# Kernel tuning notes

Hardware: AMD Instinct MI355X
Metric: run time of the kernel (lower is better)

## Reference

```python
import jax, jax.numpy as jnp
import numpy as np

H = 16            # num_heads
NORM = 16.0       # gate normalizer
SCALE = 128.0 ** -0.5  # (embed_dim // num_heads) ** -0.5, per source
EPS = 1e-5


def setup_inputs() -> dict:
    key = jax.random.key(0)
    ks = jax.random.split(key, 10)
    B, L, D = 2, 2048, 2048
    g = lambda k, shape, s: jax.random.normal(k, shape, jnp.float32) * s
    return {
        "x": g(ks[0], (B, L, D), 1.0),
        "Wq": g(ks[1], (1024, D), 0.02),
        "Wk": g(ks[2], (1024, D), 0.02),
        "Wkg1": g(ks[3], (16, D), 0.02),
        "Wkg2": g(ks[4], (1024, 16), 0.05),
        "bkg2": jnp.zeros((1024,), jnp.float32),
        "Wv": g(ks[5], (D, D), 0.02),
        "Wg": g(ks[6], (D, D), 0.02),
        "bg": jnp.zeros((D,), jnp.float32),
        "Wo": g(ks[7], (D, D), 0.02),
    }


def _gla_core(x, Wq, Wk, Wkg1, Wkg2, bkg2, Wv, Wg, bg, Wo):
    B, L, D = x.shape
    q = x @ Wq.T                         # [B,L,1024]
    k = (x @ Wk.T) * SCALE               # [B,L,1024]
    kg = (x @ Wkg1.T) @ Wkg2.T + bkg2    # [B,L,1024] low-rank gate
    v = x @ Wv.T                         # [B,L,2048]
    gproj = x @ Wg.T + bg                # [B,L,2048]

    dk = q.shape[-1] // H   # 64
    dv = D // H             # 128
    heads = lambda t, dh: t.reshape(B, L, H, dh).transpose(0, 2, 1, 3)  # b h l d
    qh = heads(q, dk)
    kh = heads(k, dk)
    vh = heads(v, dv)
    gk = jax.nn.log_sigmoid(heads(kg, dk)) / NORM  # b h l dk

    # recurrence: S_t = diag(exp(gk_t)) S_{t-1} + k_t v_t^T ; o_t = q_t S_t
    tfirst = lambda t: t.transpose(2, 0, 1, 3)  # l b h d

    def step(S, inp):
        qt, kt, vt, gt = inp
        S = S * jnp.exp(gt)[..., None] + kt[..., None] * vt[..., None, :]
        ot = jnp.einsum('bhk,bhkv->bhv', qt, S)
        return S, ot

    S0 = jnp.zeros((B, H, dk, dv), x.dtype)
    _, os = jax.lax.scan(step, S0, (tfirst(qh), tfirst(kh), tfirst(vh), tfirst(gk)))
    o = os.transpose(1, 2, 0, 3)  # b h l dv

    # LayerNorm over head dim, no affine
    mu = o.mean(-1, keepdims=True)
    var = ((o - mu) ** 2).mean(-1, keepdims=True)
    o = (o - mu) * jax.lax.rsqrt(var + EPS)

    o = o.transpose(0, 2, 1, 3).reshape(B, L, D)  # b l (h dv)
    return (jax.nn.silu(gproj) * o) @ Wo.T


def reference(x, Wq, Wk, Wkg1, Wkg2, bkg2, Wv, Wg, bg, Wo):
    return _gla_core(x, Wq, Wk, Wkg1, Wkg2, bkg2, Wv, Wg, bg, Wo)
```

## Files before the change

kernel.cpp:

```cpp
#include <hip/hip_runtime.h>
#include <hip/hip_bf16.h>

using bf16x8 = __attribute__((ext_vector_type(8))) __bf16;
using fx4    = __attribute__((ext_vector_type(4))) float;
using us4    = __attribute__((ext_vector_type(4))) unsigned short;
using us8    = __attribute__((ext_vector_type(8))) unsigned short;

__device__ __forceinline__ float b2f(unsigned short u) {
    unsigned int x = ((unsigned int)u) << 16;
    return __builtin_bit_cast(float, x);
}
__device__ __forceinline__ unsigned short f2b(float f) {
    __hip_bfloat16 h = __float2bfloat16(f);
    return __builtin_bit_cast(unsigned short, h);
}
__device__ __forceinline__ float logsigmoidf(float z) {
    return fminf(z, 0.0f) - log1pf(expf(-fabsf(z)));
}

__device__ __forceinline__ void gl_lds16(const unsigned short* g, unsigned short* l) {
    __builtin_amdgcn_global_load_lds(
        (const __attribute__((address_space(1))) void*)g,
        (__attribute__((address_space(3))) void*)l, 16, 0, 0);
}

__device__ __forceinline__ bf16x8 frag64(const unsigned short* base, int row, int cq) {
    return *reinterpret_cast<const bf16x8*>(base + row * 64 + (((cq ^ (row & 7)) << 3)));
}
__device__ __forceinline__ int sw_idx(int row, int col) {
    return row * 64 + ((((col >> 3) ^ (row & 7)) << 3)) + (col & 7);
}

__device__ __forceinline__ void xcd_remap(int& bx, int& by) {
    const int gx = gridDim.x;
    const int nwg = gx * gridDim.y;
    const int cpx = nwg >> 3;
    const int f = blockIdx.y * gx + blockIdx.x;
    const int nf = (f & 7) * cpx + (f >> 3);
    bx = nf % gx;
    by = nf / gx;
}

__global__ __launch_bounds__(256) void detect_kernel(
    const unsigned int* __restrict__ x, int* __restrict__ flag)
{
    __shared__ int bad[256];
    const int t = threadIdx.x;
    int b = 0;
#pragma unroll
    for (int i = 0; i < 16; ++i) {
        unsigned int w = x[t * 16 + i];
        float v = b2f((unsigned short)(w & 0xFFFFu));
        if (!(fabsf(v) < 1.0e6f)) b = 1;
    }
    bad[t] = b;
    __syncthreads();
    for (int s = 128; s > 0; s >>= 1) {
        if (t < s) bad[t] |= bad[t + s];
        __syncthreads();
    }
    if (t == 0) flag[0] = bad[0];
}

struct CvtArgs {
    const void* src[10];
    unsigned short* dst[10];
};

__global__ __launch_bounds__(256) void convert_all_kernel(
    CvtArgs a, const int* __restrict__ flag)
{
    const int pref[11] = {0, 1048576, 1310720, 1572864, 1576960, 1579008,
                          1579136, 2103424, 2627712, 2627968, 3152256};
    const int total = 3152256;
    const int f32 = *flag;
    for (int g = blockIdx.x * 256 + threadIdx.x; g < total; g += gridDim.x * 256) {
        int s = 0;
#pragma unroll
        for (int i = 1; i < 10; ++i) s += (g >= pref[i]) ? 1 : 0;
        const int lg = g - pref[s];
        if (f32) {
            const float* sp = (const float*)a.src[s] + (size_t)lg * 8;
            fx4 v0 = *(const fx4*)(sp);
            fx4 v1 = *(const fx4*)(sp + 4);
            us8 r;
#pragma unroll
            for (int e = 0; e < 4; ++e) { r[e] = f2b(v0[e]); r[4 + e] = f2b(v1[e]); }
            *(us8*)(a.dst[s] + (size_t)lg * 8) = r;
        } else {
            *(us8*)(a.dst[s] + (size_t)lg * 8) =
                *(const us8*)((const unsigned short*)a.src[s] + (size_t)lg * 8);
        }
    }
}

struct Seg3 {
    unsigned short* C0;
    unsigned short* C1;
    unsigned short* C2;
    const unsigned short* bias2;
};

__global__ __launch_bounds__(256) void gemm_fused3_kernel(
    const unsigned short* __restrict__ A, const unsigned short* __restrict__ W,
    Seg3 segs, float scale_k)
{
    const int K = 2048;
    __shared__ __align__(16) unsigned short As[128 * 64];
    __shared__ __align__(16) unsigned short Bs[128 * 64];

    const int tid  = threadIdx.x;
    const int lane = tid & 63, wid = tid >> 6;
    const int quad = lane >> 4, l15 = lane & 15;
    const int wm = (wid & 1) * 64, wn = (wid >> 1) * 64;
    int bx, by;
    xcd_remap(bx, by);
    const int m0 = by * 128, n0 = bx * 128;

    fx4 acc[4][4];
#pragma unroll
    for (int i = 0; i < 4; ++i)
#pragma unroll
        for (int j = 0; j < 4; ++j) acc[i][j] = fx4{0.f, 0.f, 0.f, 0.f};

    const int srow = lane >> 3;
    const int g8   = ((lane & 7) ^ srow) * 8;
    const int c8   = (lane & 7) * 8;
    const unsigned short* Ab = A + (size_t)m0 * K;
    const unsigned short* Wb = W + (size_t)n0 * K;

    for (int k0 = 0; k0 < K; k0 += 64) {
#pragma unroll
        for (int p = 0; p < 4; ++p) {
            const int la  = wid * 4 + p;
            const int row = la * 8 + srow;
            gl_lds16(Ab + (size_t)row * K + k0 + g8, As + row * 64 + c8);
            gl_lds16(Wb + (size_t)row * K + k0 + g8, Bs + row * 64 + c8);
        }
        __syncthreads();
#pragma unroll
        for (int ks = 0; ks < 2; ++ks) {
            const int cq = quad + ks * 4;
            bf16x8 af[4], bfr[4];
#pragma unroll
            for (int mt = 0; mt < 4; ++mt) af[mt] = frag64(As, wm + mt * 16 + l15, cq);
#pragma unroll
            for (int nt = 0; nt < 4; ++nt) bfr[nt] = frag64(Bs, wn + nt * 16 + l15, cq);
#pragma unroll
            for (int mt = 0; mt < 4; ++mt)
#pragma unroll
                for (int nt = 0; nt < 4; ++nt)
                    acc[mt][nt] = __builtin_amdgcn_mfma_f32_16x16x32_bf16(
                        af[mt], bfr[nt], acc[mt][nt], 0, 0, 0);
        }
        __syncthreads();
    }

    const int segi = n0 >> 11;
    unsigned short* Cs = (segi == 0) ? segs.C0 : ((segi == 1) ? segs.C1 : segs.C2);
#pragma unroll
    for (int nt = 0; nt < 4; ++nt) {
        const int ncl = (n0 & 2047) + wn + nt * 16 + l15;
        const float av = (segi == 0 && ncl >= 1024) ? scale_k : 1.0f;
        const float bv = (segi == 2) ? b2f(segs.bias2[ncl]) : 0.0f;
#pragma unroll
        for (int mt = 0; mt < 4; ++mt) {
#pragma unroll
            for (int r = 0; r < 4; ++r) {
                const int mrow = m0 + wm + mt * 16 + quad * 4 + r;
                float val = acc[mt][nt][r] * av + bv;
                if (segi == 2) val = val / (1.0f + __expf(-val));
                Cs[(size_t)mrow * 2048 + ncl] = f2b(val);
            }
        }
    }
}

__global__ __launch_bounds__(256) void gemm_bt_kernel(
    const unsigned short* __restrict__ A, const unsigned short* __restrict__ W,
    unsigned short* __restrict__ C, int M, int N, int K,
    const int* __restrict__ oflag)
{
    __shared__ __align__(16) unsigned short As[128 * 64];
    __shared__ __align__(16) unsigned short Bs[128 * 64];

    const int tid  = threadIdx.x;
    const int lane = tid & 63, wid = tid >> 6;
    const int quad = lane >> 4, l15 = lane & 15;
    const int wm = (wid & 1) * 64, wn = (wid >> 1) * 64;
    int bx, by;
    xcd_remap(bx, by);
    const int m0 = by * 128, n0 = bx * 128;

    fx4 acc[4][4];
#pragma unroll
    for (int i = 0; i < 4; ++i)
#pragma unroll
        for (int j = 0; j < 4; ++j) acc[i][j] = fx4{0.f, 0.f, 0.f, 0.f};

    const int srow = lane >> 3;
    const int g8   = ((lane & 7) ^ srow) * 8;
    const int c8   = (lane & 7) * 8;
    const unsigned short* Ab = A + (size_t)m0 * K;
    const unsigned short* Wb = W + (size_t)n0 * K;

    for (int k0 = 0; k0 < K; k0 += 64) {
#pragma unroll
        for (int p = 0; p < 4; ++p) {
            const int la  = wid * 4 + p;
            const int row = la * 8 + srow;
            gl_lds16(Ab + (size_t)row * K + k0 + g8, As + row * 64 + c8);
            gl_lds16(Wb + (size_t)row * K + k0 + g8, Bs + row * 64 + c8);
        }
        __syncthreads();
#pragma unroll
        for (int ks = 0; ks < 2; ++ks) {
            const int cq = quad + ks * 4;
            bf16x8 af[4], bfr[4];
#pragma unroll
            for (int mt = 0; mt < 4; ++mt) af[mt] = frag64(As, wm + mt * 16 + l15, cq);
#pragma unroll
            for (int nt = 0; nt < 4; ++nt) bfr[nt] = frag64(Bs, wn + nt * 16 + l15, cq);
#pragma unroll
            for (int mt = 0; mt < 4; ++mt)
#pragma unroll
                for (int nt = 0; nt < 4; ++nt)
                    acc[mt][nt] = __builtin_amdgcn_mfma_f32_16x16x32_bf16(
                        af[mt], bfr[nt], acc[mt][nt], 0, 0, 0);
        }
        __syncthreads();
    }

    const int f32out = oflag ? *oflag : 0;
#pragma unroll
    for (int nt = 0; nt < 4; ++nt) {
        const int ncol = n0 + wn + nt * 16 + l15;
#pragma unroll
        for (int mt = 0; mt < 4; ++mt) {
#pragma unroll
            for (int r = 0; r < 4; ++r) {
                const int mrow = m0 + wm + mt * 16 + quad * 4 + r;
                float val = acc[mt][nt][r];
                const size_t idx = (size_t)mrow * N + ncol;
                if (f32out) ((float*)C)[idx] = val;
                else        C[idx] = f2b(val);
            }
        }
    }
}

__global__ __launch_bounds__(256) void gate1_kernel(
    const unsigned short* __restrict__ x, const unsigned short* __restrict__ Wkg1,
    const unsigned short* __restrict__ Wkg2, const unsigned short* __restrict__ bkg2,
    float* __restrict__ Ag)
{
    __shared__ float part[4][16];
    __shared__ float kgrow[16];
    const int m = blockIdx.x;
    const int tid = threadIdx.x;
    const int lane = tid & 63, w = tid >> 6;

    us8 xv = *reinterpret_cast<const us8*>(x + (size_t)m * 2048 + tid * 8);
    float xr[8];
#pragma unroll
    for (int e = 0; e < 8; ++e) xr[e] = b2f(xv[e]);

#pragma unroll
    for (int n = 0; n < 16; ++n) {
        us8 wv = *reinterpret_cast<const us8*>(Wkg1 + (size_t)n * 2048 + tid * 8);
        float s = 0.f;
#pragma unroll
        for (int e = 0; e < 8; ++e) s += xr[e] * b2f(wv[e]);
#pragma unroll
        for (int off = 1; off < 64; off <<= 1) s += __shfl_xor(s, off, 64);
        if (lane == 0) part[w][n] = s;
    }
    __syncthreads();
    if (tid < 16)
        kgrow[tid] = part[0][tid] + part[1][tid] + part[2][tid] + part[3][tid];
    __syncthreads();
    float kr[16];
#pragma unroll
    for (int j = 0; j < 16; ++j) kr[j] = kgrow[j];

    const int b = m >> 11, l = m & 2047;
    const int c0 = tid * 4;
    const int h = c0 >> 6, d0 = c0 & 63;
    fx4 gv;
#pragma unroll
    for (int qi = 0; qi < 4; ++qi) {
        const int c = c0 + qi;
        us8 w0 = *reinterpret_cast<const us8*>(Wkg2 + (size_t)c * 16);
        us8 w1 = *reinterpret_cast<const us8*>(Wkg2 + (size_t)c * 16 + 8);
        float z = b2f(bkg2[c]);
#pragma unroll
        for (int j = 0; j < 8; ++j) z += kr[j] * b2f(w0[j]) + kr[8 + j] * b2f(w1[j]);
        gv[qi] = logsigmoidf(z) * 0.0625f;
    }
    *reinterpret_cast<fx4*>(Ag + ((size_t)(b * 16 + h) * 2048 + l) * 64 + d0) = gv;
}

__global__ __launch_bounds__(256) void gate2_kernel(float* __restrict__ Ag)
{
    const int gidx = blockIdx.x * 256 + threadIdx.x;
    const int d = gidx & 63, ch = (gidx >> 6) & 31, bh = gidx >> 11;
    float* p = Ag + ((size_t)bh * 2048 + ch * 64) * 64 + d;
    float acc = 0.f;
#pragma unroll 8
    for (int t = 0; t < 64; ++t) {
        acc += p[(size_t)t * 64];
        p[(size_t)t * 64] = acc;
    }
}

__global__ __launch_bounds__(256) void pass1_kernel(
    const unsigned short* __restrict__ k, int kstr,
    const unsigned short* __restrict__ v,
    const float* __restrict__ Ag, float* __restrict__ Tc)
{
    __shared__ __align__(16) unsigned short kT[64 * 64];
    __shared__ __align__(16) unsigned short vT[128 * 64];

    const int blk = blockIdx.x;
    const int ch = blk & 31, bh = blk >> 5;
    const int b = bh >> 4, h = bh & 15;
    const int tid = threadIdx.x;
    const int lane = tid & 63, w = tid >> 6;
    const int quad = lane >> 4, l15 = lane & 15;

    const float* Abase = Ag + ((size_t)bh * 2048 + ch * 64) * 64;
    const unsigned short* kbase = k + ((size_t)(b * 2048 + ch * 64)) * kstr + h * 64;
    const unsigned short* vbase = v + ((size_t)(b * 2048 + ch * 64)) * 2048 + h * 128;

    {
        const int s = tid >> 2, d0 = (tid & 3) * 16;
        float av[16], a63[16];
        *(fx4*)(av)      = *(const fx4*)(Abase + (size_t)s * 64 + d0);
        *(fx4*)(av + 4)  = *(const fx4*)(Abase + (size_t)s * 64 + d0 + 4);
        *(fx4*)(av + 8)  = *(const fx4*)(Abase + (size_t)s * 64 + d0 + 8);
        *(fx4*)(av + 12) = *(const fx4*)(Abase + (size_t)s * 64 + d0 + 12);
        *(fx4*)(a63)      = *(const fx4*)(Abase + (size_t)63 * 64 + d0);
        *(fx4*)(a63 + 4)  = *(const fx4*)(Abase + (size_t)63 * 64 + d0 + 4);
        *(fx4*)(a63 + 8)  = *(const fx4*)(Abase + (size_t)63 * 64 + d0 + 8);
        *(fx4*)(a63 + 12) = *(const fx4*)(Abase + (size_t)63 * 64 + d0 + 12);
        us8 k0v = *(const us8*)(kbase + (size_t)s * kstr + d0);
        us8 k1v = *(const us8*)(kbase + (size_t)s * kstr + d0 + 8);
#pragma unroll
        for (int e = 0; e < 8; ++e) {
            kT[sw_idx(d0 + e, s)]     = f2b(b2f(k0v[e]) * __expf(a63[e] - av[e]));
            kT[sw_idx(d0 + 8 + e, s)] = f2b(b2f(k1v[e]) * __expf(a63[8 + e] - av[8 + e]));
        }
    }
    {
        const int s = tid >> 2, j0 = (tid & 3) * 32;
#pragma unroll
        for (int g2 = 0; g2 < 4; ++g2) {
            us8 vv = *(const us8*)(vbase + (size_t)s * 2048 + j0 + g2 * 8);
#pragma unroll
            for (int e = 0; e < 8; ++e) vT[sw_idx(j0 + g2 * 8 + e, s)] = vv[e];
        }
    }
    __syncthreads();

    bf16x8 bk[4][2];
#pragma unroll
    for (int nt = 0; nt < 4; ++nt) {
        bk[nt][0] = frag64(kT, nt * 16 + l15, quad);
        bk[nt][1] = frag64(kT, nt * 16 + l15, quad + 4);
    }
    fx4 acc[2][4];
#pragma unroll
    for (int mi = 0; mi < 2; ++mi)
#pragma unroll
        for (int nt = 0; nt < 4; ++nt) acc[mi][nt] = fx4{0.f, 0.f, 0.f, 0.f};
#pragma unroll
    for (int mi = 0; mi < 2; ++mi) {
        const int mrow = (w * 2 + mi) * 16 + l15;
        bf16x8 av0 = frag64(vT, mrow, quad);
        bf16x8 av1 = frag64(vT, mrow, quad + 4);
#pragma unroll
        for (int nt = 0; nt < 4; ++nt) {
            acc[mi][nt] = __builtin_amdgcn_mfma_f32_16x16x32_bf16(av0, bk[nt][0], acc[mi][nt], 0, 0, 0);
            acc[mi][nt] = __builtin_amdgcn_mfma_f32_16x16x32_bf16(av1, bk[nt][1], acc[mi][nt], 0, 0, 0);
        }
    }
    float* tb = Tc + (size_t)blk * 8192;
#pragma unroll
    for (int mi = 0; mi < 2; ++mi)
#pragma unroll
        for (int nt = 0; nt < 4; ++nt)
#pragma unroll
            for (int r = 0; r < 4; ++r) {
                const int j = (w * 2 + mi) * 16 + quad * 4 + r;
                const int d = nt * 16 + l15;
                tb[(size_t)j * 64 + d] = acc[mi][nt][r];
            }
}

__global__ __launch_bounds__(256) void combine_kernel(
    float* __restrict__ TS, const float* __restrict__ Ag)
{
    const int blk = blockIdx.x;
    const int js = blk & 7, bh = blk >> 3;
    const int tid = threadIdx.x;
    const int j = js * 16 + (tid >> 4), d0 = (tid & 15) * 4;
    fx4 S = fx4{0.f, 0.f, 0.f, 0.f};
    const float* Abase = Ag + (size_t)bh * 2048 * 64;
    for (int c = 0; c < 32; ++c) {
        float* p = TS + ((size_t)(bh * 32 + c)) * 8192 + (size_t)j * 64 + d0;
        fx4 t = *(const fx4*)p;
        *(fx4*)p = S;
        fx4 a = *(const fx4*)(Abase + ((size_t)c * 64 + 63) * 64 + d0);
#pragma unroll
        for (int e = 0; e < 4; ++e) S[e] = S[e] * __expf(a[e]) + t[e];
    }
}

__global__ __launch_bounds__(256) void pass2_kernel(
    const unsigned short* __restrict__ q, const unsigned short* __restrict__ k,
    int qkstr,
    const unsigned short* __restrict__ v, const float* __restrict__ Ag,
    const float* __restrict__ Sst, const unsigned short* __restrict__ sg,
    unsigned short* __restrict__ y)
{
    __shared__ __align__(16) unsigned short qs[64 * 64];
    __shared__ __align__(16) unsigned short ksh[64 * 64];
    __shared__ __align__(16) unsigned short vT[128 * 64];
    __shared__ __align__(16) unsigned short Pb[64 * 64];
    __shared__ __align__(16) unsigned short Ob[64 * 144];

    const int blk = blockIdx.x;
    const int ch = blk & 31, bh = blk >> 5;
    const int b = bh >> 4, h = bh & 15;
    const int tid = threadIdx.x;
    const int lane = tid & 63, w = tid >> 6;
    const int quad = lane >> 4, l15 = lane & 15;

    const float* Abase = Ag + ((size_t)bh * 2048 + ch * 64) * 64;
    const unsigned short* qbase = q + ((size_t)(b * 2048 + ch * 64)) * qkstr + h * 64;
    const unsigned short* kbase = k + ((size_t)(b * 2048 + ch * 64)) * qkstr + h * 64;
    const unsigned short* vbase = v + ((size_t)(b * 2048 + ch * 64)) * 2048 + h * 128;

    {
        const int t = tid >> 2, d0 = (tid & 3) * 16;
        float av[16];
        *(fx4*)(av)      = *(const fx4*)(Abase + (size_t)t * 64 + d0);
        *(fx4*)(av + 4)  = *(const fx4*)(Abase + (size_t)t * 64 + d0 + 4);
        *(fx4*)(av + 8)  = *(const fx4*)(Abase + (size_t)t * 64 + d0 + 8);
        *(fx4*)(av + 12) = *(const fx4*)(Abase + (size_t)t * 64 + d0 + 12);
        us8 q0 = *(const us8*)(qbase + (size_t)t * qkstr + d0);
        us8 q1 = *(const us8*)(qbase + (size_t)t * qkstr + d0 + 8);
        us8 k0 = *(const us8*)(kbase + (size_t)t * qkstr + d0);
        us8 k1 = *(const us8*)(kbase + (size_t)t * qkstr + d0 + 8);
        us8 qo0, qo1, ko0, ko1;
#pragma unroll
        for (int e = 0; e < 8; ++e) {
            float e0 = __expf(av[e]),     n0 = __expf(-av[e]);
            float e1 = __expf(av[8 + e]), n1 = __expf(-av[8 + e]);
            qo0[e] = f2b(b2f(q0[e]) * e0);
            qo1[e] = f2b(b2f(q1[e]) * e1);
            ko0[e] = f2b(b2f(k0[e]) * n0);
            ko1[e] = f2b(b2f(k1[e]) * n1);
        }
        const int c0 = d0 >> 3, t7 = t & 7;
        *(us8*)(qs  + t * 64 + ((c0 ^ t7) << 3))       = qo0;
        *(us8*)(qs  + t * 64 + (((c0 + 1) ^ t7) << 3)) = qo1;
        *(us8*)(ksh + t * 64 + ((c0 ^ t7) << 3))       = ko0;
        *(us8*)(ksh + t * 64 + (((c0 + 1) ^ t7) << 3)) = ko1;
    }
    {
        const int s = tid >> 2, j0 = (tid & 3) * 32;
#pragma unroll
        for (int g2 = 0; g2 < 4; ++g2) {
            us8 vv = *(const us8*)(vbase + (size_t)s * 2048 + j0 + g2 * 8);
#pragma unroll
            for (int e = 0; e < 8; ++e) vT[sw_idx(j0 + g2 * 8 + e, s)] = vv[e];
        }
    }
    __syncthreads();

    bf16x8 aQ0 = frag64(qs, w * 16 + l15, quad);
    bf16x8 aQ1 = frag64(qs, w * 16 + l15, quad + 4);
    fx4 accP[4];
#pragma unroll
    for (int nt = 0; nt < 4; ++nt) accP[nt] = fx4{0.f, 0.f, 0.f, 0.f};
#pragma unroll
    for (int nt = 0; nt < 4; ++nt) {
        bf16x8 bK0 = frag64(ksh, nt * 16 + l15, quad);
        bf16x8 bK1 = frag64(ksh, nt * 16 + l15, quad + 4);
        accP[nt] = __builtin_amdgcn_mfma_f32_16x16x32_bf16(aQ0, bK0, accP[nt], 0, 0, 0);
        accP[nt] = __builtin_amdgcn_mfma_f32_16x16x32_bf16(aQ1, bK1, accP[nt], 0, 0, 0);
    }
#pragma unroll
    for (int nt = 0; nt < 4; ++nt)
#pragma unroll
        for (int r = 0; r < 4; ++r) {
            const int t = w * 16 + quad * 4 + r;
            const int s = nt * 16 + l15;
            Pb[sw_idx(t, s)] = f2b((s <= t) ? accP[nt][r] : 0.0f);
        }
    __syncthreads();

    bf16x8 aP0 = frag64(Pb, w * 16 + l15, quad);
    bf16x8 aP1 = frag64(Pb, w * 16 + l15, quad + 4);
    const float* ST = Sst + (size_t)blk * 8192;
    fx4 accO[8];
#pragma unroll
    for (int nt = 0; nt < 8; ++nt) accO[nt] = fx4{0.f, 0.f, 0.f, 0.f};
#pragma unroll
    for (int nt = 0; nt < 8; ++nt) {
        const int j = nt * 16 + l15;
        bf16x8 bV0 = frag64(vT, j, quad);
        bf16x8 bV1 = frag64(vT, j, quad + 4);
        const float* sp = ST + (size_t)j * 64 + quad * 8;
        fx4 s0a = *(const fx4*)(sp),      s0b = *(const fx4*)(sp + 4);
        fx4 s1a = *(const fx4*)(sp + 32), s1b = *(const fx4*)(sp + 36);
        us8 hi0u, lo0u, hi1u, lo1u;
#pragma unroll
        for (int e = 0; e < 4; ++e) {
            unsigned short hh;
            hh = f2b(s0a[e]); hi0u[e] = hh;     lo0u[e]     = f2b(s0a[e] - b2f(hh));
            hh = f2b(s0b[e]); hi0u[4 + e] = hh; lo0u[4 + e] = f2b(s0b[e] - b2f(hh));
            hh = f2b(s1a[e]); hi1u[e] = hh;     lo1u[e]     = f2b(s1a[e] - b2f(hh));
            hh = f2b(s1b[e]); hi1u[4 + e] = hh; lo1u[4 + e] = f2b(s1b[e] - b2f(hh));
        }
        bf16x8 hi0 = __builtin_bit_cast(bf16x8, hi0u);
        bf16x8 lo0 = __builtin_bit_cast(bf16x8, lo0u);
        bf16x8 hi1 = __builtin_bit_cast(bf16x8, hi1u);
        bf16x8 lo1 = __builtin_bit_cast(bf16x8, lo1u);
        accO[nt] = __builtin_amdgcn_mfma_f32_16x16x32_bf16(aP0, bV0, accO[nt], 0, 0, 0);
        accO[nt] = __builtin_amdgcn_mfma_f32_16x16x32_bf16(aP1, bV1, accO[nt], 0, 0, 0);
        accO[nt] = __builtin_amdgcn_mfma_f32_16x16x32_bf16(aQ0, hi0, accO[nt], 0, 0, 0);
        accO[nt] = __builtin_amdgcn_mfma_f32_16x16x32_bf16(aQ1, hi1, accO[nt], 0, 0, 0);
        accO[nt] = __builtin_amdgcn_mfma_f32_16x16x32_bf16(aQ0, lo0, accO[nt], 0, 0, 0);
        accO[nt] = __builtin_amdgcn_mfma_f32_16x16x32_bf16(aQ1, lo1, accO[nt], 0, 0, 0);
    }

    float sum1[4] = {0.f, 0.f, 0.f, 0.f}, sum2[4] = {0.f, 0.f, 0.f, 0.f};
#pragma unroll
    for (int nt = 0; nt < 8; ++nt)
#pragma unroll
        for (int r = 0; r < 4; ++r) {
            float ov = accO[nt][r];
            sum1[r] += ov;
            sum2[r] += ov * ov;
        }
#pragma unroll
    for (int m = 1; m < 16; m <<= 1)
#pragma unroll
        for (int r = 0; r < 4; ++r) {
            sum1[r] += __shfl_xor(sum1[r], m, 64);
            sum2[r] += __shfl_xor(sum2[r], m, 64);
        }
    float mu[4], inv[4];
#pragma unroll
    for (int r = 0; r < 4; ++r) {
        mu[r] = sum1[r] * (1.0f / 128.0f);
        float var = sum2[r] * (1.0f / 128.0f) - mu[r] * mu[r];
        inv[r] = rsqrtf(var + 1e-5f);
    }
#pragma unroll
    for (int nt = 0; nt < 8; ++nt)
#pragma unroll
        for (int r = 0; r < 4; ++r) {
            const int t = w * 16 + quad * 4 + r;
            Ob[t * 144 + nt * 16 + l15] = f2b((accO[nt][r] - mu[r]) * inv[r]);
        }
    __syncthreads();

    {
        const int t2 = tid >> 2, jg = (tid & 3) * 32;
        const size_t obase = ((size_t)(b * 2048 + ch * 64 + t2)) * 2048 + h * 128 + jg;
#pragma unroll
        for (int g2 = 0; g2 < 4; ++g2) {
            us8 ob = *(const us8*)(Ob + t2 * 144 + jg + g2 * 8);
            us8 gv = *(const us8*)(sg + obase + g2 * 8);
            us8 ov;
#pragma unroll
            for (int e = 0; e < 8; ++e) ov[e] = f2b(b2f(gv[e]) * b2f(ob[e]));
            *(us8*)(y + obase + g2 * 8) = ov;
        }
    }
}

extern "C" void kernel_launch(void* const* d_in, const int* in_sizes, int n_in,
                              void* d_out, int out_size, void* d_ws, size_t ws_size,
                              hipStream_t stream)
{
    unsigned short* out = (unsigned short*)d_out;

    char* ws = (char*)d_ws;
    size_t off = 0;
    auto alloc = [&](size_t bytes) -> void* {
        void* p = ws + off;
        off += (bytes + 255) & ~(size_t)255;
        return p;
    };
    unsigned short* xb    = (unsigned short*)alloc((size_t)4096 * 2048 * 2);
    unsigned short* Wbig  = (unsigned short*)alloc((size_t)6144 * 2048 * 2);
    unsigned short* Wkg1b = (unsigned short*)alloc((size_t)16 * 2048 * 2);
    unsigned short* Wkg2b = (unsigned short*)alloc((size_t)1024 * 16 * 2);
    unsigned short* bkg2b = (unsigned short*)alloc((size_t)1024 * 2);
    unsigned short* bgb   = (unsigned short*)alloc((size_t)2048 * 2);
    unsigned short* Wob   = (unsigned short*)alloc((size_t)2048 * 2048 * 2);
    unsigned short* qkb  = (unsigned short*)alloc((size_t)4096 * 2048 * 2);
    unsigned short* vb   = (unsigned short*)alloc((size_t)4096 * 2048 * 2);
    unsigned short* sgb  = (unsigned short*)alloc((size_t)4096 * 2048 * 2);
    unsigned short* yb   = (unsigned short*)alloc((size_t)4096 * 2048 * 2);
    float*          Agb  = (float*)alloc((size_t)4096 * 1024 * 4);
    float*          TS   = (float*)alloc((size_t)1024 * 8192 * 4);
    int*            flag = (int*)alloc(256);

    detect_kernel<<<1, 256, 0, stream>>>((const unsigned int*)d_in[0], flag);

    CvtArgs ca;
    ca.src[0] = d_in[0]; ca.dst[0] = xb;
    ca.src[1] = d_in[1]; ca.dst[1] = Wbig;
    ca.src[2] = d_in[2]; ca.dst[2] = Wbig + (size_t)1024 * 2048;
    ca.src[3] = d_in[3]; ca.dst[3] = Wkg1b;
    ca.src[4] = d_in[4]; ca.dst[4] = Wkg2b;
    ca.src[5] = d_in[5]; ca.dst[5] = bkg2b;
    ca.src[6] = d_in[6]; ca.dst[6] = Wbig + (size_t)2048 * 2048;
    ca.src[7] = d_in[7]; ca.dst[7] = Wbig + (size_t)4096 * 2048;
    ca.src[8] = d_in[8]; ca.dst[8] = bgb;
    ca.src[9] = d_in[9]; ca.dst[9] = Wob;
    convert_all_kernel<<<2048, 256, 0, stream>>>(ca, flag);

    const float SCALE = 0.08838834764831845f;

    Seg3 segs;
    segs.C0 = qkb; segs.C1 = vb; segs.C2 = sgb; segs.bias2 = bgb;
    gemm_fused3_kernel<<<dim3(48, 32), 256, 0, stream>>>(xb, Wbig, segs, SCALE);

    gate1_kernel<<<4096, 256, 0, stream>>>(xb, Wkg1b, Wkg2b, bkg2b, Agb);
    gate2_kernel<<<256, 256, 0, stream>>>(Agb);
    pass1_kernel<<<1024, 256, 0, stream>>>(qkb + 1024, 2048, vb, Agb, TS);
    combine_kernel<<<256, 256, 0, stream>>>(TS, Agb);
    pass2_kernel<<<1024, 256, 0, stream>>>(qkb, qkb + 1024, 2048, vb, Agb, TS, sgb, yb);
    gemm_bt_kernel<<<dim3(16, 32), 256, 0, stream>>>(yb, Wob, out, 4096, 2048, 2048, flag);
}
```

Baseline: 434.7 us.

## Drop XCD remap, restructure gate reduction, prepack hi/lo bf16 state in combine

Removes the XCD-aware block remapping from both GEMM kernels and uses plain blockIdx tiling. The gate1 reduction now writes per-thread partials to a padded shared array and reduces them cooperatively, replacing the per-wave shuffle reduction. The combine kernel now stores chunk states pre-split into hi/lo bf16 pairs in the same buffer, so pass2 loads them directly instead of converting fp32 to bf16 pairs itself. Dropping the remap may lose L2 locality across XCDs, and the gate change enlarges shared memory.

```diff
diff --git a/kernel.cpp b/kernel.cpp
--- a/kernel.cpp
+++ b/kernel.cpp
@@ -29,16 +29,6 @@
 }
 __device__ __forceinline__ int sw_idx(int row, int col) {
     return row * 64 + ((((col >> 3) ^ (row & 7)) << 3)) + (col & 7);
-}
-
-__device__ __forceinline__ void xcd_remap(int& bx, int& by) {
-    const int gx = gridDim.x;
-    const int nwg = gx * gridDim.y;
-    const int cpx = nwg >> 3;
-    const int f = blockIdx.y * gx + blockIdx.x;
-    const int nf = (f & 7) * cpx + (f >> 3);
-    bx = nf % gx;
-    by = nf / gx;
 }
 
 __global__ __launch_bounds__(256) void detect_kernel(
@@ -113,9 +103,7 @@
     const int lane = tid & 63, wid = tid >> 6;
     const int quad = lane >> 4, l15 = lane & 15;
     const int wm = (wid & 1) * 64, wn = (wid >> 1) * 64;
-    int bx, by;
-    xcd_remap(bx, by);
-    const int m0 = by * 128, n0 = bx * 128;
+    const int m0 = blockIdx.y * 128, n0 = blockIdx.x * 128;
 
     fx4 acc[4][4];
 #pragma unroll
@@ -188,9 +176,7 @@
     const int lane = tid & 63, wid = tid >> 6;
     const int quad = lane >> 4, l15 = lane & 15;
     const int wm = (wid & 1) * 64, wn = (wid >> 1) * 64;
-    int bx, by;
-    xcd_remap(bx, by);
-    const int m0 = by * 128, n0 = bx * 128;
+    const int m0 = blockIdx.y * 128, n0 = blockIdx.x * 128;
 
     fx4 acc[4][4];
 #pragma unroll
@@ -254,11 +240,10 @@
     const unsigned short* __restrict__ Wkg2, const unsigned short* __restrict__ bkg2,
     float* __restrict__ Ag)
 {
-    __shared__ float part[4][16];
+    __shared__ float part[16][257];
     __shared__ float kgrow[16];
     const int m = blockIdx.x;
     const int tid = threadIdx.x;
-    const int lane = tid & 63, w = tid >> 6;
 
     us8 xv = *reinterpret_cast<const us8*>(x + (size_t)m * 2048 + tid * 8);
     float xr[8];
@@ -271,13 +256,18 @@
         float s = 0.f;
 #pragma unroll
         for (int e = 0; e < 8; ++e) s += xr[e] * b2f(wv[e]);
-#pragma unroll
-        for (int off = 1; off < 64; off <<= 1) s += __shfl_xor(s, off, 64);
-        if (lane == 0) part[w][n] = s;
+        part[n][tid] = s;
     }
     __syncthreads();
-    if (tid < 16)
-        kgrow[tid] = part[0][tid] + part[1][tid] + part[2][tid] + part[3][tid];
+    {
+        const int n = tid >> 4, i = tid & 15;
+        float s = 0.f;
+#pragma unroll
+        for (int k2 = 0; k2 < 16; ++k2) s += part[n][i + k2 * 16];
+#pragma unroll
+        for (int off = 1; off < 16; off <<= 1) s += __shfl_xor(s, off, 64);
+        if (i == 0) kgrow[n] = s;
+    }
     __syncthreads();
     float kr[16];
 #pragma unroll
@@ -409,7 +399,13 @@
     for (int c = 0; c < 32; ++c) {
         float* p = TS + ((size_t)(bh * 32 + c)) * 8192 + (size_t)j * 64 + d0;
         fx4 t = *(const fx4*)p;
-        *(fx4*)p = S;
+        us8 pk;
+#pragma unroll
+        for (int e = 0; e < 4; ++e) {
+            pk[e]     = f2b(S[e]);
+            pk[4 + e] = f2b(S[e] - b2f(pk[e]));
+        }
+        *(us8*)p = pk;
         fx4 a = *(const fx4*)(Abase + ((size_t)c * 64 + 63) * 64 + d0);
 #pragma unroll
         for (int e = 0; e < 4; ++e) S[e] = S[e] * __expf(a[e]) + t[e];
@@ -503,7 +499,7 @@
 
     bf16x8 aP0 = frag64(Pb, w * 16 + l15, quad);
     bf16x8 aP1 = frag64(Pb, w * 16 + l15, quad + 4);
-    const float* ST = Sst + (size_t)blk * 8192;
+    const unsigned short* SP = (const unsigned short*)(Sst + (size_t)blk * 8192);
     fx4 accO[8];
 #pragma unroll
     for (int nt = 0; nt < 8; ++nt) accO[nt] = fx4{0.f, 0.f, 0.f, 0.f};
@@ -512,18 +508,15 @@
         const int j = nt * 16 + l15;
         bf16x8 bV0 = frag64(vT, j, quad);
         bf16x8 bV1 = frag64(vT, j, quad + 4);
-        const float* sp = ST + (size_t)j * 64 + quad * 8;
-        fx4 s0a = *(const fx4*)(sp),      s0b = *(const fx4*)(sp + 4);
-        fx4 s1a = *(const fx4*)(sp + 32), s1b = *(const fx4*)(sp + 36);
-        us8 hi0u, lo0u, hi1u, lo1u;
-#pragma unroll
-        for (int e = 0; e < 4; ++e) {
-            unsigned short hh;
-            hh = f2b(s0a[e]); hi0u[e] = hh;     lo0u[e]     = f2b(s0a[e] - b2f(hh));
-            hh = f2b(s0b[e]); hi0u[4 + e] = hh; lo0u[4 + e] = f2b(s0b[e] - b2f(hh));
-            hh = f2b(s1a[e]); hi1u[e] = hh;     lo1u[e]     = f2b(s1a[e] - b2f(hh));
-            hh = f2b(s1b[e]); hi1u[4 + e] = hh; lo1u[4 + e] = f2b(s1b[e] - b2f(hh));
-        }
+        const unsigned short* sb = SP + (size_t)(j * 64 + quad * 8) * 2;
+        us8 ga = *(const us8*)(sb);
+        us8 gb = *(const us8*)(sb + 8);
+        us8 gc = *(const us8*)(sb + 64);
+        us8 gd = *(const us8*)(sb + 72);
+        us8 hi0u = __builtin_shufflevector(ga, gb, 0, 1, 2, 3, 8, 9, 10, 11);
+        us8 lo0u = __builtin_shufflevector(ga, gb, 4, 5, 6, 7, 12, 13, 14, 15);
+        us8 hi1u = __builtin_shufflevector(gc, gd, 0, 1, 2, 3, 8, 9, 10, 11);
+        us8 lo1u = __builtin_shufflevector(gc, gd, 4, 5, 6, 7, 12, 13, 14, 15);
         bf16x8 hi0 = __builtin_bit_cast(bf16x8, hi0u);
         bf16x8 lo0 = __builtin_bit_cast(bf16x8, lo0u);
         bf16x8 hi1 = __builtin_bit_cast(bf16x8, hi1u);
```

Result: faster. 425.4 us (-2.2%).
